# Performance work log

Measured on AMD Instinct MI355X. Metric: run time of the kernel, lower is better.

The kernel has to match this reference:

```python
import jax, jax.numpy as jnp
import numpy as np

N, M, D = 32768, 4096, 512  # batch, m*n prototypes, prototype dim


def setup_inputs() -> dict:
    key = jax.random.key(0)
    k1, k2 = jax.random.split(key)
    z = jax.random.normal(k1, (N, D), dtype=jnp.float32)
    prototypes = jax.random.normal(k2, (M, D), dtype=jnp.float32)
    return {"z": z, "prototypes": prototypes}


def reference(z, prototypes):
    # Squared euclidean distances via GEMM expansion:
    #   ||z - p||^2 = ||z||^2 - 2 z.p + ||p||^2
    z2 = jnp.sum(z * z, axis=1, keepdims=True)            # [N,1]
    p2 = jnp.sum(prototypes * prototypes, axis=1)         # [M]
    d2 = z2 - 2.0 * (z @ prototypes.T) + p2[None, :]      # [N,M]
    min_idx = jnp.argmin(d2, axis=1)                      # same argmin as cdist
    winner_prototypes = prototypes[min_idx]               # [N,D]
    return winner_prototypes, min_idx
```

## Files before the change

### kernel.cpp

```cpp
#include <hip/hip_runtime.h>


#define N_ROWS 32768
#define M_PROTO 4096
#define DIM 512

typedef _Float16 half8 __attribute__((ext_vector_type(8)));
typedef _Float16 half4_t __attribute__((ext_vector_type(4)));
typedef float f32x4 __attribute__((ext_vector_type(4)));

__device__ __forceinline__ void gl_lds16(const void* g, void* l) {
    __builtin_amdgcn_global_load_lds(
        (const __attribute__((address_space(1))) unsigned int*)g,
        (__attribute__((address_space(3))) unsigned int*)l, 16, 0, 0);
}

__global__ __launch_bounds__(256) void p2_kernel(const float* __restrict__ p,
                                                 float* __restrict__ p2) {
    const int w = threadIdx.x >> 6, l = threadIdx.x & 63;
    const int m = blockIdx.x * 4 + w;
    const float4* p4 = (const float4*)p + (size_t)m * 128;
    float s = 0.f;
#pragma unroll
    for (int i = 0; i < 2; ++i) {
        float4 v = p4[l * 2 + i];
        s += v.x * v.x + v.y * v.y + v.z * v.z + v.w * v.w;
    }
#pragma unroll
    for (int mm = 1; mm < 64; mm <<= 1) s += __shfl_xor(s, mm);
    if (l == 0) p2[m] = s;
}

__global__ __launch_bounds__(256) void conv_p_kernel(const float* __restrict__ p,
                                                     _Float16* __restrict__ ph,
                                                     _Float16* __restrict__ pl) {
    const int tile = blockIdx.x;
    const int bi = tile >> 3, kt = tile & 7;
    const float4* p4 = (const float4*)p;
    const size_t tb = (size_t)tile * 8192;
#pragma unroll
    for (int it = 0; it < 8; ++it) {
        int q = it * 256 + threadIdx.x;
        int row = q >> 4, kq = q & 15;
        float4 v = p4[(size_t)(bi * 128 + row) * 128 + kt * 16 + kq];
        _Float16 h0 = (_Float16)v.x, h1 = (_Float16)v.y;
        _Float16 h2 = (_Float16)v.z, h3 = (_Float16)v.w;
        half4_t hv = {h0, h1, h2, h3};
        half4_t lv = {(_Float16)(v.x - (float)h0), (_Float16)(v.y - (float)h1),
                      (_Float16)(v.z - (float)h2), (_Float16)(v.w - (float)h3)};
        int addr = row * 64 + (((kq >> 1) ^ (row & 7)) << 3) + ((kq & 1) << 2);
        *(half4_t*)&ph[tb + addr] = hv;
        *(half4_t*)&pl[tb + addr] = lv;
    }
}

__global__ __launch_bounds__(256) void conv_z_kernel(const float* __restrict__ z,
                                                     half8* __restrict__ zh,
                                                     half8* __restrict__ zl) {
    const float4* z4 = (const float4*)z;
#pragma unroll
    for (int it = 0; it < 8; ++it) {
        int slot = it * 262144 + blockIdx.x * 256 + threadIdx.x;
        int lane = slot & 63, sk = slot >> 6;
        int c = lane & 15, g = (lane >> 4) & 3;
        int S = sk >> 4, ks = sk & 15;
        int rowi = S * 16 + c;
        float4 v0 = z4[(size_t)rowi * 128 + ks * 8 + g * 2 + 0];
        float4 v1 = z4[(size_t)rowi * 128 + ks * 8 + g * 2 + 1];
        float x0 = -2.f * v0.x, x1 = -2.f * v0.y, x2 = -2.f * v0.z, x3 = -2.f * v0.w;
        float x4 = -2.f * v1.x, x5 = -2.f * v1.y, x6 = -2.f * v1.z, x7 = -2.f * v1.w;
        _Float16 h0 = (_Float16)x0, h1 = (_Float16)x1, h2 = (_Float16)x2, h3 = (_Float16)x3;
        _Float16 h4 = (_Float16)x4, h5 = (_Float16)x5, h6 = (_Float16)x6, h7 = (_Float16)x7;
        half8 hv = {h0, h1, h2, h3, h4, h5, h6, h7};
        half8 lv = {(_Float16)(x0 - (float)h0), (_Float16)(x1 - (float)h1),
                    (_Float16)(x2 - (float)h2), (_Float16)(x3 - (float)h3),
                    (_Float16)(x4 - (float)h4), (_Float16)(x5 - (float)h5),
                    (_Float16)(x6 - (float)h6), (_Float16)(x7 - (float)h7)};
        zh[slot] = hv;
        zl[slot] = lv;
    }
}

__global__ __launch_bounds__(512, 2) void som_main(
    const half8* __restrict__ zh, const half8* __restrict__ zl,
    const _Float16* __restrict__ ph, const _Float16* __restrict__ pl,
    const float* __restrict__ p2, const float* __restrict__ prot,
    float* __restrict__ out) {
    __shared__ __align__(16) _Float16 sPH[2][8192];
    __shared__ __align__(16) _Float16 sPL[2][8192];
    __shared__ int sFI[128];

    const int tid = threadIdx.x;
    const int w = tid >> 6, l = tid & 63;
    const int g = l >> 4, c = l & 15;
    const int blk = blockIdx.x, brow = blk * 128;
    const int S = blk * 8 + w;

    half8 za[16], zb[16];
#pragma unroll
    for (int ks = 0; ks < 16; ++ks) {
        size_t slot = (size_t)(S * 16 + ks) * 64 + l;
        za[ks] = zh[slot];
        zb[ks] = zl[slot];
    }

    {
        const int lo = l * 8;
#pragma unroll
        for (int j = 0; j < 2; ++j) {
            int c0 = (w * 2 + j) * 512;
            gl_lds16(ph + c0 + lo, &sPH[0][c0]);
            gl_lds16(pl + c0 + lo, &sPL[0][c0]);
        }
    }
    __syncthreads();

    float minv[4];
    int mini[4];
#pragma unroll
    for (int r = 0; r < 4; ++r) { minv[r] = 3.0e38f; mini[r] = 0; }

    for (int bi = 0; bi < 32; ++bi) {
        f32x4 acc[8];
#pragma unroll
        for (int jt = 0; jt < 8; ++jt) acc[jt] = (f32x4){0.f, 0.f, 0.f, 0.f};

#pragma unroll
        for (int kt = 0; kt < 8; ++kt) {
            const int cur = kt & 1;
            const int tp = bi * 8 + kt;
            if (tp < 255) {
                const _Float16* sph = ph + (size_t)(tp + 1) * 8192;
                const _Float16* spl = pl + (size_t)(tp + 1) * 8192;
                const int lo = l * 8;
#pragma unroll
                for (int j = 0; j < 2; ++j) {
                    int c0 = (w * 2 + j) * 512;
                    gl_lds16(sph + c0 + lo, &sPH[cur ^ 1][c0]);
                    gl_lds16(spl + c0 + lo, &sPL[cur ^ 1][c0]);
                }
            }
#pragma unroll
            for (int ksl = 0; ksl < 2; ++ksl) {
                const int ks = kt * 2 + ksl;
#pragma unroll
                for (int jt = 0; jt < 8; ++jt) {
                    int row = jt * 16 + c;
                    int addr = row * 64 + (((ksl * 4 + g) ^ (row & 7)) << 3);
                    half8 bh = *(half8*)&sPH[cur][addr];
                    half8 bl = *(half8*)&sPL[cur][addr];
                    acc[jt] = __builtin_amdgcn_mfma_f32_16x16x32_f16(za[ks], bh, acc[jt], 0, 0, 0);
                    acc[jt] = __builtin_amdgcn_mfma_f32_16x16x32_f16(za[ks], bl, acc[jt], 0, 0, 0);
                    acc[jt] = __builtin_amdgcn_mfma_f32_16x16x32_f16(zb[ks], bh, acc[jt], 0, 0, 0);
                }
            }
            __syncthreads();
        }

#pragma unroll
        for (int jt = 0; jt < 8; ++jt) {
            int colg = bi * 128 + jt * 16 + c;
            float pv = p2[colg];
#pragma unroll
            for (int r = 0; r < 4; ++r) {
                float s = acc[jt][r] + pv;
                if (s < minv[r] || (s == minv[r] && colg < mini[r])) {
                    minv[r] = s;
                    mini[r] = colg;
                }
            }
        }
    }

#pragma unroll
    for (int r = 0; r < 4; ++r) {
        float v = minv[r];
        int id = mini[r];
#pragma unroll
        for (int mm = 1; mm < 16; mm <<= 1) {
            float ov = __shfl_xor(v, mm);
            int oi = __shfl_xor(id, mm);
            if (ov < v || (ov == v && oi < id)) { v = ov; id = oi; }
        }
        if (c == 0) {
            int rl = w * 16 + g * 4 + r;
            sFI[rl] = id;
            out[(size_t)N_ROWS * DIM + brow + rl] = (float)id;
        }
    }
    __syncthreads();

    const float4* pr4 = (const float4*)prot;
    float4* out4 = (float4*)out;
#pragma unroll 4
    for (int it = 0; it < 32; ++it) {
        int q = it * 512 + tid;
        int row = q >> 7, qk = q & 127;
        int fi = sFI[row];
        out4[(size_t)(brow + row) * 128 + qk] = pr4[(size_t)fi * 128 + qk];
    }
}

__global__ __launch_bounds__(256) void som_fallback(const float* __restrict__ z,
                                                    const float* __restrict__ prot,
                                                    const float* __restrict__ p2,
                                                    float* __restrict__ out) {
    __shared__ __align__(16) _Float16 sZH[64 * 64];
    __shared__ __align__(16) _Float16 sZL[64 * 64];
    __shared__ __align__(16) _Float16 sPH[128 * 64];
    __shared__ __align__(16) _Float16 sPL[128 * 64];
    __shared__ float sMV[4][64];
    __shared__ int sMI[4][64];
    __shared__ int sFI[64];

    const int tid = threadIdx.x;
    const int w = tid >> 6, l = tid & 63;
    const int g = l >> 4, c = l & 15;
    const int brow = blockIdx.x * 64;
    const float4* z4 = (const float4*)z;
    const float4* pr4 = (const float4*)prot;

    float minv[4][4];
    int mini[4][4];
#pragma unroll
    for (int i = 0; i < 4; ++i)
#pragma unroll
        for (int r = 0; r < 4; ++r) { minv[i][r] = 3.0e38f; mini[i][r] = 0; }

    for (int bcol = 0; bcol < M_PROTO; bcol += 128) {
        f32x4 acc[4][2];
#pragma unroll
        for (int i = 0; i < 4; ++i)
#pragma unroll
            for (int jt = 0; jt < 2; ++jt) acc[i][jt] = (f32x4){0.f, 0.f, 0.f, 0.f};
        for (int kt = 0; kt < 8; ++kt) {
            __syncthreads();
#pragma unroll
            for (int it = 0; it < 4; ++it) {
                int q = it * 256 + tid;
                int row = q >> 4, kq = q & 15;
                float4 v = z4[(size_t)(brow + row) * 128 + kt * 16 + kq];
                float x0 = -2.f * v.x, x1 = -2.f * v.y, x2 = -2.f * v.z, x3 = -2.f * v.w;
                _Float16 h0 = (_Float16)x0, h1 = (_Float16)x1;
                _Float16 h2 = (_Float16)x2, h3 = (_Float16)x3;
                half4_t hv = {h0, h1, h2, h3};
                half4_t lv = {(_Float16)(x0 - (float)h0), (_Float16)(x1 - (float)h1),
                              (_Float16)(x2 - (float)h2), (_Float16)(x3 - (float)h3)};
                int addr = row * 64 + (((kq >> 1) ^ (row & 7)) << 3) + ((kq & 1) << 2);
                *(half4_t*)&sZH[addr] = hv;
                *(half4_t*)&sZL[addr] = lv;
            }
#pragma unroll
            for (int it = 0; it < 8; ++it) {
                int q = it * 256 + tid;
                int row = q >> 4, kq = q & 15;
                float4 v = pr4[(size_t)(bcol + row) * 128 + kt * 16 + kq];
                _Float16 h0 = (_Float16)v.x, h1 = (_Float16)v.y;
                _Float16 h2 = (_Float16)v.z, h3 = (_Float16)v.w;
                half4_t hv = {h0, h1, h2, h3};
                half4_t lv = {(_Float16)(v.x - (float)h0), (_Float16)(v.y - (float)h1),
                              (_Float16)(v.z - (float)h2), (_Float16)(v.w - (float)h3)};
                int addr = row * 64 + (((kq >> 1) ^ (row & 7)) << 3) + ((kq & 1) << 2);
                *(half4_t*)&sPH[addr] = hv;
                *(half4_t*)&sPL[addr] = lv;
            }
            __syncthreads();
#pragma unroll
            for (int ks = 0; ks < 2; ++ks) {
                half8 ah[4], al[4], bh[2], bl[2];
#pragma unroll
                for (int i = 0; i < 4; ++i) {
                    int row = i * 16 + c;
                    int addr = row * 64 + (((ks * 4 + g) ^ (row & 7)) << 3);
                    ah[i] = *(half8*)&sZH[addr];
                    al[i] = *(half8*)&sZL[addr];
                }
#pragma unroll
                for (int jt = 0; jt < 2; ++jt) {
                    int row = w * 32 + jt * 16 + c;
                    int addr = row * 64 + (((ks * 4 + g) ^ (row & 7)) << 3);
                    bh[jt] = *(half8*)&sPH[addr];
                    bl[jt] = *(half8*)&sPL[addr];
                }
#pragma unroll
                for (int i = 0; i < 4; ++i)
#pragma unroll
                    for (int jt = 0; jt < 2; ++jt) {
                        acc[i][jt] = __builtin_amdgcn_mfma_f32_16x16x32_f16(ah[i], bh[jt], acc[i][jt], 0, 0, 0);
                        acc[i][jt] = __builtin_amdgcn_mfma_f32_16x16x32_f16(ah[i], bl[jt], acc[i][jt], 0, 0, 0);
                        acc[i][jt] = __builtin_amdgcn_mfma_f32_16x16x32_f16(al[i], bh[jt], acc[i][jt], 0, 0, 0);
                    }
            }
        }
#pragma unroll
        for (int jt = 0; jt < 2; ++jt) {
            int colg = bcol + w * 32 + jt * 16 + c;
            float pv = p2[colg];
#pragma unroll
            for (int i = 0; i < 4; ++i)
#pragma unroll
                for (int r = 0; r < 4; ++r) {
                    float s = acc[i][jt][r] + pv;
                    if (s < minv[i][r] || (s == minv[i][r] && colg < mini[i][r])) {
                        minv[i][r] = s;
                        mini[i][r] = colg;
                    }
                }
        }
    }
#pragma unroll
    for (int i = 0; i < 4; ++i)
#pragma unroll
        for (int r = 0; r < 4; ++r) {
            float v = minv[i][r];
            int id = mini[i][r];
#pragma unroll
            for (int mm = 1; mm < 16; mm <<= 1) {
                float ov = __shfl_xor(v, mm);
                int oi = __shfl_xor(id, mm);
                if (ov < v || (ov == v && oi < id)) { v = ov; id = oi; }
            }
            if (c == 0) {
                sMV[w][i * 16 + g * 4 + r] = v;
                sMI[w][i * 16 + g * 4 + r] = id;
            }
        }
    __syncthreads();
    if (tid < 64) {
        float v = sMV[0][tid];
        int id = sMI[0][tid];
#pragma unroll
        for (int ww = 1; ww < 4; ++ww) {
            float ov = sMV[ww][tid];
            int oi = sMI[ww][tid];
            if (ov < v || (ov == v && oi < id)) { v = ov; id = oi; }
        }
        sFI[tid] = id;
        out[(size_t)N_ROWS * DIM + brow + tid] = (float)id;
    }
    __syncthreads();
    float4* out4 = (float4*)out;
#pragma unroll 4
    for (int it = 0; it < 32; ++it) {
        int q = it * 256 + tid;
        int row = q >> 7, qk = q & 127;
        int fi = sFI[row];
        out4[(size_t)(brow + row) * 128 + qk] = pr4[(size_t)fi * 128 + qk];
    }
}

extern "C" void kernel_launch(void* const* d_in, const int* in_sizes, int n_in,
                              void* d_out, int out_size, void* d_ws, size_t ws_size,
                              hipStream_t stream) {
    const float* z = (const float*)d_in[0];
    const float* prot = (const float*)d_in[1];
    char* base = (char*)d_ws;
    float* p2 = (float*)base;

    const size_t NEED = 16384
                      + 8388608
                      + 67108864;

    p2_kernel<<<M_PROTO / 4, 256, 0, stream>>>(prot, p2);

    if (ws_size >= NEED) {
        _Float16* ph = (_Float16*)(base + 16384);
        _Float16* pl = (_Float16*)(base + 16384 + 4194304);
        half8* zh = (half8*)(base + 16384 + 8388608);
        half8* zl = (half8*)(base + 16384 + 8388608 + 33554432);
        conv_p_kernel<<<256, 256, 0, stream>>>(prot, ph, pl);
        conv_z_kernel<<<1024, 256, 0, stream>>>(z, zh, zl);
        som_main<<<N_ROWS / 128, 512, 0, stream>>>(zh, zl, ph, pl, p2, prot, (float*)d_out);
    } else {
        som_fallback<<<N_ROWS / 64, 256, 0, stream>>>(z, prot, p2, (float*)d_out);
    }
}
```

Baseline: 527.8 us.

## Fuse z split-conversion into main kernel and give each wave two row strips

Removes the separate conv_z kernel and its 64 MB workspace round-trip: the main kernel now loads fp32 z rows itself and splits them into fp16 hi/lo fragments in registers. Blocks shrink to 256 threads, with each wave owning two 16-row strips so every LDS prototype fragment feeds twice as many MFMAs. This halves LDS read traffic per MFMA and avoids writing then rereading z in global memory. The cost is roughly doubled register use (two sets of A fragments and accumulators) and lower occupancy (launch bounds 256,1), which may expose latency.

```diff
diff --git a/kernel.cpp b/kernel.cpp
--- a/kernel.cpp
+++ b/kernel.cpp
@@ -54,35 +54,8 @@
     }
 }
 
-__global__ __launch_bounds__(256) void conv_z_kernel(const float* __restrict__ z,
-                                                     half8* __restrict__ zh,
-                                                     half8* __restrict__ zl) {
-    const float4* z4 = (const float4*)z;
-#pragma unroll
-    for (int it = 0; it < 8; ++it) {
-        int slot = it * 262144 + blockIdx.x * 256 + threadIdx.x;
-        int lane = slot & 63, sk = slot >> 6;
-        int c = lane & 15, g = (lane >> 4) & 3;
-        int S = sk >> 4, ks = sk & 15;
-        int rowi = S * 16 + c;
-        float4 v0 = z4[(size_t)rowi * 128 + ks * 8 + g * 2 + 0];
-        float4 v1 = z4[(size_t)rowi * 128 + ks * 8 + g * 2 + 1];
-        float x0 = -2.f * v0.x, x1 = -2.f * v0.y, x2 = -2.f * v0.z, x3 = -2.f * v0.w;
-        float x4 = -2.f * v1.x, x5 = -2.f * v1.y, x6 = -2.f * v1.z, x7 = -2.f * v1.w;
-        _Float16 h0 = (_Float16)x0, h1 = (_Float16)x1, h2 = (_Float16)x2, h3 = (_Float16)x3;
-        _Float16 h4 = (_Float16)x4, h5 = (_Float16)x5, h6 = (_Float16)x6, h7 = (_Float16)x7;
-        half8 hv = {h0, h1, h2, h3, h4, h5, h6, h7};
-        half8 lv = {(_Float16)(x0 - (float)h0), (_Float16)(x1 - (float)h1),
-                    (_Float16)(x2 - (float)h2), (_Float16)(x3 - (float)h3),
-                    (_Float16)(x4 - (float)h4), (_Float16)(x5 - (float)h5),
-                    (_Float16)(x6 - (float)h6), (_Float16)(x7 - (float)h7)};
-        zh[slot] = hv;
-        zl[slot] = lv;
-    }
-}
-
-__global__ __launch_bounds__(512, 2) void som_main(
-    const half8* __restrict__ zh, const half8* __restrict__ zl,
+__global__ __launch_bounds__(256, 1) void som_main(
+    const float* __restrict__ z,
     const _Float16* __restrict__ ph, const _Float16* __restrict__ pl,
     const float* __restrict__ p2, const float* __restrict__ prot,
     float* __restrict__ out) {
@@ -94,36 +67,51 @@
     const int w = tid >> 6, l = tid & 63;
     const int g = l >> 4, c = l & 15;
     const int blk = blockIdx.x, brow = blk * 128;
-    const int S = blk * 8 + w;
-
-    half8 za[16], zb[16];
-#pragma unroll
-    for (int ks = 0; ks < 16; ++ks) {
-        size_t slot = (size_t)(S * 16 + ks) * 64 + l;
-        za[ks] = zh[slot];
-        zb[ks] = zl[slot];
-    }
-
-    {
-        const int lo = l * 8;
-#pragma unroll
-        for (int j = 0; j < 2; ++j) {
-            int c0 = (w * 2 + j) * 512;
-            gl_lds16(ph + c0 + lo, &sPH[0][c0]);
-            gl_lds16(pl + c0 + lo, &sPL[0][c0]);
-        }
+
+    half8 za[2][16], zb[2][16];
+#pragma unroll
+    for (int st = 0; st < 2; ++st) {
+        const int rowg = brow + (w * 2 + st) * 16 + c;
+        const float4* zr = (const float4*)z + (size_t)rowg * 128;
+#pragma unroll
+        for (int ks = 0; ks < 16; ++ks) {
+            float4 v0 = zr[ks * 8 + g * 2 + 0];
+            float4 v1 = zr[ks * 8 + g * 2 + 1];
+            float x0 = -2.f * v0.x, x1 = -2.f * v0.y, x2 = -2.f * v0.z, x3 = -2.f * v0.w;
+            float x4 = -2.f * v1.x, x5 = -2.f * v1.y, x6 = -2.f * v1.z, x7 = -2.f * v1.w;
+            _Float16 h0 = (_Float16)x0, h1 = (_Float16)x1, h2 = (_Float16)x2, h3 = (_Float16)x3;
+            _Float16 h4 = (_Float16)x4, h5 = (_Float16)x5, h6 = (_Float16)x6, h7 = (_Float16)x7;
+            half8 hv = {h0, h1, h2, h3, h4, h5, h6, h7};
+            half8 lv = {(_Float16)(x0 - (float)h0), (_Float16)(x1 - (float)h1),
+                        (_Float16)(x2 - (float)h2), (_Float16)(x3 - (float)h3),
+                        (_Float16)(x4 - (float)h4), (_Float16)(x5 - (float)h5),
+                        (_Float16)(x6 - (float)h6), (_Float16)(x7 - (float)h7)};
+            za[st][ks] = hv;
+            zb[st][ks] = lv;
+        }
+    }
+
+#pragma unroll
+    for (int j = 0; j < 4; ++j) {
+        const int off = j * 2048 + tid * 8;
+        gl_lds16(ph + off, &sPH[0][off]);
+        gl_lds16(pl + off, &sPL[0][off]);
     }
     __syncthreads();
 
-    float minv[4];
-    int mini[4];
-#pragma unroll
-    for (int r = 0; r < 4; ++r) { minv[r] = 3.0e38f; mini[r] = 0; }
+    float minv[2][4];
+    int mini[2][4];
+#pragma unroll
+    for (int st = 0; st < 2; ++st)
+#pragma unroll
+        for (int r = 0; r < 4; ++r) { minv[st][r] = 3.0e38f; mini[st][r] = 0; }
 
     for (int bi = 0; bi < 32; ++bi) {
-        f32x4 acc[8];
-#pragma unroll
-        for (int jt = 0; jt < 8; ++jt) acc[jt] = (f32x4){0.f, 0.f, 0.f, 0.f};
+        f32x4 acc[2][8];
+#pragma unroll
+        for (int st = 0; st < 2; ++st)
+#pragma unroll
+            for (int jt = 0; jt < 8; ++jt) acc[st][jt] = (f32x4){0.f, 0.f, 0.f, 0.f};
 
 #pragma unroll
         for (int kt = 0; kt < 8; ++kt) {
@@ -132,12 +120,11 @@
             if (tp < 255) {
                 const _Float16* sph = ph + (size_t)(tp + 1) * 8192;
                 const _Float16* spl = pl + (size_t)(tp + 1) * 8192;
-                const int lo = l * 8;
-#pragma unroll
-                for (int j = 0; j < 2; ++j) {
-                    int c0 = (w * 2 + j) * 512;
-                    gl_lds16(sph + c0 + lo, &sPH[cur ^ 1][c0]);
-                    gl_lds16(spl + c0 + lo, &sPL[cur ^ 1][c0]);
+#pragma unroll
+                for (int j = 0; j < 4; ++j) {
+                    const int off = j * 2048 + tid * 8;
+                    gl_lds16(sph + off, &sPH[cur ^ 1][off]);
+                    gl_lds16(spl + off, &sPL[cur ^ 1][off]);
                 }
             }
 #pragma unroll
@@ -145,13 +132,16 @@
                 const int ks = kt * 2 + ksl;
 #pragma unroll
                 for (int jt = 0; jt < 8; ++jt) {
-                    int row = jt * 16 + c;
-                    int addr = row * 64 + (((ksl * 4 + g) ^ (row & 7)) << 3);
+                    const int row = jt * 16 + c;
+                    const int addr = row * 64 + (((ksl * 4 + g) ^ (row & 7)) << 3);
                     half8 bh = *(half8*)&sPH[cur][addr];
                     half8 bl = *(half8*)&sPL[cur][addr];
-                    acc[jt] = __builtin_amdgcn_mfma_f32_16x16x32_f16(za[ks], bh, acc[jt], 0, 0, 0);
-                    acc[jt] = __builtin_amdgcn_mfma_f32_16x16x32_f16(za[ks], bl, acc[jt], 0, 0, 0);
-                    acc[jt] = __builtin_amdgcn_mfma_f32_16x16x32_f16(zb[ks], bh, acc[jt], 0, 0, 0);
+#pragma unroll
+                    for (int st = 0; st < 2; ++st) {
+                        acc[st][jt] = __builtin_amdgcn_mfma_f32_16x16x32_f16(za[st][ks], bh, acc[st][jt], 0, 0, 0);
+                        acc[st][jt] = __builtin_amdgcn_mfma_f32_16x16x32_f16(za[st][ks], bl, acc[st][jt], 0, 0, 0);
+                        acc[st][jt] = __builtin_amdgcn_mfma_f32_16x16x32_f16(zb[st][ks], bh, acc[st][jt], 0, 0, 0);
+                    }
                 }
             }
             __syncthreads();
@@ -159,44 +149,48 @@
 
 #pragma unroll
         for (int jt = 0; jt < 8; ++jt) {
-            int colg = bi * 128 + jt * 16 + c;
+            const int colg = bi * 128 + jt * 16 + c;
             float pv = p2[colg];
 #pragma unroll
-            for (int r = 0; r < 4; ++r) {
-                float s = acc[jt][r] + pv;
-                if (s < minv[r] || (s == minv[r] && colg < mini[r])) {
-                    minv[r] = s;
-                    mini[r] = colg;
-                }
-            }
-        }
-    }
-
-#pragma unroll
-    for (int r = 0; r < 4; ++r) {
-        float v = minv[r];
-        int id = mini[r];
-#pragma unroll
-        for (int mm = 1; mm < 16; mm <<= 1) {
-            float ov = __shfl_xor(v, mm);
-            int oi = __shfl_xor(id, mm);
-            if (ov < v || (ov == v && oi < id)) { v = ov; id = oi; }
-        }
-        if (c == 0) {
-            int rl = w * 16 + g * 4 + r;
-            sFI[rl] = id;
-            out[(size_t)N_ROWS * DIM + brow + rl] = (float)id;
-        }
-    }
+            for (int st = 0; st < 2; ++st)
+#pragma unroll
+                for (int r = 0; r < 4; ++r) {
+                    float s = acc[st][jt][r] + pv;
+                    if (s < minv[st][r] || (s == minv[st][r] && colg < mini[st][r])) {
+                        minv[st][r] = s;
+                        mini[st][r] = colg;
+                    }
+                }
+        }
+    }
+
+#pragma unroll
+    for (int st = 0; st < 2; ++st)
+#pragma unroll
+        for (int r = 0; r < 4; ++r) {
+            float v = minv[st][r];
+            int id = mini[st][r];
+#pragma unroll
+            for (int mm = 1; mm < 16; mm <<= 1) {
+                float ov = __shfl_xor(v, mm);
+                int oi = __shfl_xor(id, mm);
+                if (ov < v || (ov == v && oi < id)) { v = ov; id = oi; }
+            }
+            if (c == 0) {
+                const int rl = (w * 2 + st) * 16 + g * 4 + r;
+                sFI[rl] = id;
+                out[(size_t)N_ROWS * DIM + brow + rl] = (float)id;
+            }
+        }
     __syncthreads();
 
     const float4* pr4 = (const float4*)prot;
     float4* out4 = (float4*)out;
 #pragma unroll 4
-    for (int it = 0; it < 32; ++it) {
-        int q = it * 512 + tid;
-        int row = q >> 7, qk = q & 127;
-        int fi = sFI[row];
+    for (int it = 0; it < 64; ++it) {
+        const int q = it * 256 + tid;
+        const int row = q >> 7, qk = q & 127;
+        const int fi = sFI[row];
         out4[(size_t)(brow + row) * 128 + qk] = pr4[(size_t)fi * 128 + qk];
     }
 }
@@ -357,20 +351,15 @@
     char* base = (char*)d_ws;
     float* p2 = (float*)base;
 
-    const size_t NEED = 16384
-                      + 8388608
-                      + 67108864;
+    const size_t NEED = 16384 + 8388608;
 
     p2_kernel<<<M_PROTO / 4, 256, 0, stream>>>(prot, p2);
 
     if (ws_size >= NEED) {
         _Float16* ph = (_Float16*)(base + 16384);
         _Float16* pl = (_Float16*)(base + 16384 + 4194304);
-        half8* zh = (half8*)(base + 16384 + 8388608);
-        half8* zl = (half8*)(base + 16384 + 8388608 + 33554432);
         conv_p_kernel<<<256, 256, 0, stream>>>(prot, ph, pl);
-        conv_z_kernel<<<1024, 256, 0, stream>>>(z, zh, zl);
-        som_main<<<N_ROWS / 128, 512, 0, stream>>>(zh, zl, ph, pl, p2, prot, (float*)d_out);
+        som_main<<<N_ROWS / 128, 256, 0, stream>>>(z, ph, pl, p2, prot, (float*)d_out);
     } else {
         som_fallback<<<N_ROWS / 64, 256, 0, stream>>>(z, prot, p2, (float*)d_out);
     }
```

Result: slower. 574.8 us (+8.9%).
